# Performance work log

Measured on AMD Instinct MI355X. Metric: run time of the kernel, lower is better.

## Reference

```python
import jax, jax.numpy as jnp
import numpy as np

N_HEAD = 12

def setup_inputs() -> dict:
    key = jax.random.key(0)
    k1, k2, k3, k4, k5 = jax.random.split(key, 5)
    B, T, C = 16, 1024, 768
    s = 0.02
    return {
        "x": jax.random.normal(k1, (B, T, C), dtype=jnp.float32),
        "W_attn": jax.random.normal(k2, (C, 3 * C), dtype=jnp.float32) * s,
        "b_attn": jax.random.normal(k3, (3 * C,), dtype=jnp.float32) * s,
        "W_proj": jax.random.normal(k4, (C, C), dtype=jnp.float32) * s,
        "b_proj": jax.random.normal(k5, (C,), dtype=jnp.float32) * s,
    }

def reference(x, W_attn, b_attn, W_proj, b_proj):
    B, T, C = x.shape
    H = N_HEAD
    d = C // H
    qkv = x @ W_attn + b_attn                      # [B,T,3C]
    q, k, v = jnp.split(qkv, 3, axis=-1)
    # [B,H,T,d]
    q = q.reshape(B, T, H, d).transpose(0, 2, 1, 3)
    k = k.reshape(B, T, H, d).transpose(0, 2, 1, 3)
    v = v.reshape(B, T, H, d).transpose(0, 2, 1, 3)
    scale = 1.0 / jnp.sqrt(jnp.array(d, dtype=x.dtype))
    att = jnp.einsum('bhqd,bhkd->bhqk', q, k) * scale   # [B,H,T,T]
    causal = jnp.tril(jnp.ones((T, T), dtype=bool))
    att = jnp.where(causal[None, None], att, -jnp.inf)
    att = jax.nn.softmax(att, axis=-1)
    # dropout is identity in eval mode (p=0 for deterministic reference)
    y = jnp.einsum('bhqk,bhkd->bhqd', att, v)            # [B,H,T,d]
    y = y.transpose(0, 2, 1, 3).reshape(B, T, C)
    return y @ W_proj + b_proj
```

## Files before the change

kernel.cpp:

```cpp
#include <hip/hip_runtime.h>
#include <cstddef>


typedef __bf16 bf16_t;
typedef __bf16 bf16x4 __attribute__((ext_vector_type(4)));
typedef __bf16 bf16x8 __attribute__((ext_vector_type(8)));
typedef float  f32x4  __attribute__((ext_vector_type(4)));

#define MFMA16(a,b,c) __builtin_amdgcn_mfma_f32_16x16x32_bf16((a),(b),(c),0,0,0)
#define GLOAD16(gp, lp) \
  __builtin_amdgcn_global_load_lds((const __attribute__((address_space(1))) unsigned int*)(gp), \
                                   (__attribute__((address_space(3))) unsigned int*)(lp), 16, 0, 0)

#define SWZ(row, c) (((row) * 64) + ((((c) ^ ((row) & 7)) * 8)))

#define QSCALE 0.1803368801111f

__global__ __launch_bounds__(256)
void prep_kernel(const float* __restrict__ x, bf16_t* __restrict__ Xb,
                 const float* __restrict__ Wa, bf16_t* __restrict__ WaT,
                 const float* __restrict__ Wp, bf16_t* __restrict__ WpT)
{
    __shared__ bf16_t tile[32][33];
    const int bx = blockIdx.x;
    if (bx < 12288) {
        const size_t i = ((size_t)bx * 256 + threadIdx.x) * 4;
        float4 f = *(const float4*)(x + i);
        bf16x4 o = {(bf16_t)f.x, (bf16_t)f.y, (bf16_t)f.z, (bf16_t)f.w};
        *(bf16x4*)(Xb + i) = o;
        return;
    }
    const float* in;  bf16_t* out;  int R, Cn, c0, r0;
    if (bx < 14016) {
        const int t = bx - 12288;
        in = Wa; out = WaT; R = 768; Cn = 2304;
        c0 = (t % 72) * 32; r0 = (t / 72) * 32;
    } else {
        const int t = bx - 14016;
        in = Wp; out = WpT; R = 768; Cn = 768;
        c0 = (t % 24) * 32; r0 = (t / 24) * 32;
    }
    const int tx = threadIdx.x & 31, ty = threadIdx.x >> 5;
#pragma unroll
    for (int i = 0; i < 4; ++i)
        tile[ty + i*8][tx] = (bf16_t)in[(size_t)(r0 + ty + i*8) * Cn + c0 + tx];
    __syncthreads();
#pragma unroll
    for (int i = 0; i < 4; ++i)
        out[(size_t)(c0 + ty + i*8) * R + r0 + tx] = tile[tx][ty + i*8];
}

#define LGKM0() asm volatile("s_waitcnt lgkmcnt(0)" ::: "memory")
#define VMC(n)  asm volatile("s_waitcnt vmcnt(" #n ")" ::: "memory")
#define PBAR()  __builtin_amdgcn_s_barrier()
#define PRIO1() __builtin_amdgcn_s_setprio(1)
#define PRIO0() __builtin_amdgcn_s_setprio(0)

#define STAGE_HT(buf, kt, ht) do { \
    const int r0_ = w * 16 + (((ht) & 1) ? 128 : 0); \
    if ((ht) < 2) { \
        GLOAD16(WT + (size_t)(nt + r0_ + lr) * 768 + (kt) + lcs,     &Bs[buf][r0_ * 64]); \
        GLOAD16(WT + (size_t)(nt + r0_ + 8 + lr) * 768 + (kt) + lcs, &Bs[buf][(r0_ + 8) * 64]); \
    } else { \
        GLOAD16(Xb + (size_t)(mt + r0_ + lr) * 768 + (kt) + lcs,     &As[buf][r0_ * 64]); \
        GLOAD16(Xb + (size_t)(mt + r0_ + 8 + lr) * 768 + (kt) + lcs, &As[buf][(r0_ + 8) * 64]); \
    } \
} while (0)

#define RD_BX(dst, buf) do { \
    _Pragma("unroll") for (int j_ = 0; j_ < 4; ++j_) \
    _Pragma("unroll") for (int ks_ = 0; ks_ < 2; ++ks_) \
        (dst)[j_][ks_] = *(const bf16x8*)(&As[buf][SWZ(wc * 64 + j_ * 16 + lm, ks_ * 4 + lq)]); \
} while (0)

#define RD_AW(dst, buf, F0, NF) do { \
    _Pragma("unroll") for (int p_ = 0; p_ < (NF); ++p_) \
    _Pragma("unroll") for (int ks_ = 0; ks_ < 2; ++ks_) \
        (dst)[p_][ks_] = *(const bf16x8*)(&Bs[buf][SWZ(wr * 128 + ((F0) + p_) * 16 + lm, ks_ * 4 + lq)]); \
} while (0)

#define MFMA_Q(AW, BX, F0) do { \
    _Pragma("unroll") for (int ks_ = 0; ks_ < 2; ++ks_) \
    _Pragma("unroll") for (int p_ = 0; p_ < 2; ++p_) \
    _Pragma("unroll") for (int j_ = 0; j_ < 4; ++j_) \
        acc[(F0) + p_][j_] = MFMA16((AW)[p_][ks_], (BX)[j_][ks_], acc[(F0) + p_][j_]); \
} while (0)

__global__ __launch_bounds__(512)
void qkv_gemm8(const bf16_t* __restrict__ Xb, const bf16_t* __restrict__ WT,
               const float* __restrict__ bias,
               bf16_t* __restrict__ Qb, bf16_t* __restrict__ Kb, bf16_t* __restrict__ VT)
{
    __shared__ bf16_t As[2][256 * 64];
    __shared__ bf16_t Bs[2][256 * 64];
    const int tid = threadIdx.x;
    const int w = tid >> 6, l = tid & 63;
    const int lm = l & 15, lq = l >> 4;
    const int lr = l >> 3;
    const int lcs = ((l & 7) ^ lr) * 8;
    const int wr = w >> 2, wc = w & 3;

    const int g = blockIdx.x;
    const int gt = (g & 7) * 72 + (g >> 3);
    const int bm = gt / 9, bn = gt % 9;
    const int mt = bm * 256, nt = bn * 256;

    f32x4 acc[8][4];
    const f32x4 z4 = {0.f, 0.f, 0.f, 0.f};
#pragma unroll
    for (int i = 0; i < 8; ++i)
#pragma unroll
        for (int j = 0; j < 4; ++j) acc[i][j] = z4;

    bf16x8 bx0[4][2], bx1[4][2];
    bf16x8 aw0[2][2], aw12[4][2], aw3[2][2];

    STAGE_HT(0, 0, 0); STAGE_HT(0, 0, 1); STAGE_HT(0, 0, 2); STAGE_HT(0, 0, 3);
    STAGE_HT(1, 64, 0); STAGE_HT(1, 64, 1);
    VMC(4);
    PBAR();
    RD_BX(bx0, 0); RD_AW(aw0, 0, 0, 2);

#pragma unroll 1
    for (int it = 0; it < 5; ++it) {
        const int kv = it * 128 + 64, ku2 = kv + 64, kv2 = ku2 + 64;
        RD_AW(aw12, 0, 2, 4);
        STAGE_HT(1, kv, 2);
        PBAR(); LGKM0();
        PRIO1(); MFMA_Q(aw0, bx0, 0); PRIO0();
        PBAR();
        RD_AW(aw3, 0, 6, 2);
        STAGE_HT(1, kv, 3);
        PBAR(); LGKM0();
        PRIO1(); MFMA_Q(aw12, bx0, 2); PRIO0();
        PBAR();
        STAGE_HT(0, ku2, 0);
        PBAR();
        PRIO1(); MFMA_Q(&aw12[2], bx0, 4); PRIO0();
        VMC(2);
        PBAR();
        RD_BX(bx1, 1); RD_AW(aw0, 1, 0, 2);
        STAGE_HT(0, ku2, 1);
        PBAR(); LGKM0();
        PRIO1(); MFMA_Q(aw3, bx0, 6); PRIO0();
        PBAR();
        RD_AW(aw12, 1, 2, 4);
        STAGE_HT(0, ku2, 2);
        PBAR(); LGKM0();
        PRIO1(); MFMA_Q(aw0, bx1, 0); PRIO0();
        PBAR();
        RD_AW(aw3, 1, 6, 2);
        STAGE_HT(0, ku2, 3);
        PBAR(); LGKM0();
        PRIO1(); MFMA_Q(aw12, bx1, 2); PRIO0();
        PBAR();
        STAGE_HT(1, kv2, 0);
        PBAR();
        PRIO1(); MFMA_Q(&aw12[2], bx1, 4); PRIO0();
        VMC(2);
        PBAR();
        RD_BX(bx0, 0); RD_AW(aw0, 0, 0, 2);
        STAGE_HT(1, kv2, 1);
        PBAR(); LGKM0();
        PRIO1(); MFMA_Q(aw3, bx1, 6); PRIO0();
        PBAR();
    }

    RD_AW(aw12, 0, 2, 4);
    STAGE_HT(1, 704, 2);
    PBAR(); LGKM0();
    PRIO1(); MFMA_Q(aw0, bx0, 0); PRIO0();
    PBAR();
    RD_AW(aw3, 0, 6, 2);
    STAGE_HT(1, 704, 3);
    PBAR(); LGKM0();
    PRIO1(); MFMA_Q(aw12, bx0, 2); PRIO0();
    PBAR();
    PRIO1(); MFMA_Q(&aw12[2], bx0, 4); PRIO0();
    VMC(0);
    PBAR();
    RD_BX(bx1, 1); RD_AW(aw0, 1, 0, 2);
    MFMA_Q(aw3, bx0, 6);
    RD_AW(aw12, 1, 2, 4);
    LGKM0();
    MFMA_Q(aw0, bx1, 0);
    MFMA_Q(aw12, bx1, 2);
    RD_AW(aw3, 1, 6, 2);
    LGKM0();
    MFMA_Q(&aw12[2], bx1, 4);
    MFMA_Q(aw3, bx1, 6);

    const int which = (nt) / 768;
    const int b_ = mt >> 10;
    const int tb = (mt & 1023) + wc * 64;
    if (which == 2) {
#pragma unroll
        for (int f = 0; f < 8; ++f) {
            const int nglob = nt + wr * 128 + f * 16 + lq * 4;
            const int nin = nglob - 1536;
            const int h = nin >> 6, d0 = nin & 63;
            bf16_t* vt = VT + (size_t)(b_ * 12 + h) * 65536;
            const float4 bv = *(const float4*)(bias + nglob);
#pragma unroll
            for (int j = 0; j < 4; ++j) {
                const int t = tb + j * 16 + lm;
                f32x4 v = acc[f][j];
                vt[(size_t)(d0 + 0) * 1024 + t] = (bf16_t)(v[0] + bv.x);
                vt[(size_t)(d0 + 1) * 1024 + t] = (bf16_t)(v[1] + bv.y);
                vt[(size_t)(d0 + 2) * 1024 + t] = (bf16_t)(v[2] + bv.z);
                vt[(size_t)(d0 + 3) * 1024 + t] = (bf16_t)(v[3] + bv.w);
            }
        }
    } else {
        bf16_t* dst = (which == 0) ? Qb : Kb;
        const float qs = (which == 0) ? QSCALE : 1.0f;
#pragma unroll
        for (int f = 0; f < 8; ++f) {
            const int nglob = nt + wr * 128 + f * 16 + lq * 4;
            const int nin = nglob - which * 768;
            const int h = nin >> 6, d0 = nin & 63;
            const float4 bv = *(const float4*)(bias + nglob);
#pragma unroll
            for (int j = 0; j < 4; ++j) {
                const int t = tb + j * 16 + lm;
                f32x4 v = acc[f][j];
                bf16x4 o4 = {(bf16_t)((v[0] + bv.x) * qs), (bf16_t)((v[1] + bv.y) * qs),
                             (bf16_t)((v[2] + bv.z) * qs), (bf16_t)((v[3] + bv.w) * qs)};
                *(bf16x4*)(dst + ((size_t)(b_ * 12 + h) * 1024 + t) * 64 + d0) = o4;
            }
        }
    }
}

__global__ __launch_bounds__(256, 3)
void attn_kernel(const bf16_t* __restrict__ Qb, const bf16_t* __restrict__ Kb,
                 const bf16_t* __restrict__ VT, bf16_t* __restrict__ Y)
{
    __shared__ bf16_t Ks[2][64 * 64];
    __shared__ bf16_t Vs[2][64 * 64];
    __shared__ bf16_t Plds[4 * 16 * 72];
    const int tid = threadIdx.x;
    const int w = tid >> 6, l = tid & 63;
    const int lm = l & 15, lq = l >> 4;
    const int lr = l >> 3;
    const int lc8 = ((l & 7) ^ lr) * 8;
    const int xp = blockIdx.x;
    const int bh = blockIdx.y;
    const int loq = xp * 128, hiq = (7 - xp) * 128;

    int qmin[4];
    qmin[0] = loq + w * 32;      qmin[1] = qmin[0] + 16;
    qmin[2] = hiq + w * 32;      qmin[3] = qmin[2] + 16;

    const bf16_t* Kbase = Kb + (size_t)bh * 65536;
    const bf16_t* Vbase = VT + (size_t)bh * 65536;
    bf16_t* Pw = &Plds[w * 1152];
    const int r0a = w * 16, r0b = w * 16 + 8;

    bf16x8 bq[4][2];
#pragma unroll
    for (int m = 0; m < 4; ++m) {
        const bf16_t* Qp = Qb + ((size_t)bh * 1024 + qmin[m] + lm) * 64;
        bq[m][0] = *(const bf16x8*)(Qp + lq * 8);
        bq[m][1] = *(const bf16x8*)(Qp + 32 + lq * 8);
    }

    f32x4 O[4][4];
    float li[4] = {0.f, 0.f, 0.f, 0.f};
    const f32x4 z4 = {0.f, 0.f, 0.f, 0.f};
#pragma unroll
    for (int m = 0; m < 4; ++m)
#pragma unroll
        for (int s = 0; s < 4; ++s) O[m][s] = z4;

    const int kend = hiq + 64;

    GLOAD16(Kbase + (size_t)(r0a + lr) * 64 + lc8,   &Ks[0][r0a * 64]);
    GLOAD16(Kbase + (size_t)(r0b + lr) * 64 + lc8,   &Ks[0][r0b * 64]);
    GLOAD16(Vbase + (size_t)(r0a + lr) * 1024 + lc8, &Vs[0][r0a * 64]);
    GLOAD16(Vbase + (size_t)(r0b + lr) * 1024 + lc8, &Vs[0][r0b * 64]);
    __syncthreads();

    int cb = 0;
    for (int k0 = 0; k0 <= kend; k0 += 64) {
        const int nxt = cb ^ 1;
        if (k0 + 64 <= kend) {
            const int kn = k0 + 64;
            if (nxt) {
                GLOAD16(Kbase + (size_t)(kn + r0a + lr) * 64 + lc8,        &Ks[1][r0a * 64]);
                GLOAD16(Kbase + (size_t)(kn + r0b + lr) * 64 + lc8,        &Ks[1][r0b * 64]);
                GLOAD16(Vbase + (size_t)(r0a + lr) * 1024 + kn + lc8,      &Vs[1][r0a * 64]);
                GLOAD16(Vbase + (size_t)(r0b + lr) * 1024 + kn + lc8,      &Vs[1][r0b * 64]);
            } else {
                GLOAD16(Kbase + (size_t)(kn + r0a + lr) * 64 + lc8,        &Ks[0][r0a * 64]);
                GLOAD16(Kbase + (size_t)(kn + r0b + lr) * 64 + lc8,        &Ks[0][r0b * 64]);
                GLOAD16(Vbase + (size_t)(r0a + lr) * 1024 + kn + lc8,      &Vs[0][r0a * 64]);
                GLOAD16(Vbase + (size_t)(r0b + lr) * 1024 + kn + lc8,      &Vs[0][r0b * 64]);
            }
        }
        const bf16_t* Kc = Ks[cb];
        const bf16_t* Vc = Vs[cb];
#pragma unroll
        for (int m = 0; m < 4; ++m) {
            if (k0 > qmin[m] + 15) continue;
            f32x4 S[4];
#pragma unroll
            for (int s = 0; s < 4; ++s) S[s] = z4;
#pragma unroll
            for (int ks = 0; ks < 2; ++ks)
#pragma unroll
                for (int s = 0; s < 4; ++s) {
                    bf16x8 ak = *(const bf16x8*)(&Kc[SWZ(s * 16 + lm, ks * 4 + lq)]);
                    S[s] = MFMA16(ak, bq[m][ks], S[s]);
                }
            if (k0 + 63 > qmin[m]) {
                const int q = qmin[m] + lm;
#pragma unroll
                for (int s = 0; s < 4; ++s)
#pragma unroll
                    for (int rg = 0; rg < 4; ++rg)
                        if (k0 + s * 16 + lq * 4 + rg > q) S[s][rg] = -1e30f;
            }
            float ls = 0.f;
#pragma unroll
            for (int s = 0; s < 4; ++s)
#pragma unroll
                for (int rg = 0; rg < 4; ++rg) {
                    float pv = exp2f(S[s][rg]);
                    S[s][rg] = pv;
                    ls += pv;
                }
            li[m] += ls;
#pragma unroll
            for (int s = 0; s < 4; ++s) {
                bf16x4 p4 = {(bf16_t)S[s][0], (bf16_t)S[s][1],
                             (bf16_t)S[s][2], (bf16_t)S[s][3]};
                *(bf16x4*)(&Pw[lm * 72 + s * 16 + lq * 4]) = p4;
            }
#pragma unroll
            for (int ks = 0; ks < 2; ++ks) {
                bf16x8 bp = *(const bf16x8*)(&Pw[lm * 72 + ks * 32 + lq * 8]);
#pragma unroll
                for (int s = 0; s < 4; ++s) {
                    bf16x8 av = *(const bf16x8*)(&Vc[SWZ(s * 16 + lm, ks * 4 + lq)]);
                    O[m][s] = MFMA16(av, bp, O[m][s]);
                }
            }
        }
        __syncthreads();
        cb = nxt;
    }

    const int b = bh / 12, h = bh % 12;
#pragma unroll
    for (int m = 0; m < 4; ++m) {
        float s0 = li[m];
        s0 += __shfl_xor(s0, 16, 64);
        s0 += __shfl_xor(s0, 32, 64);
        const float inv = 1.f / s0;
        const size_t row = ((size_t)(b * 1024 + qmin[m] + lm)) * 768 + h * 64;
#pragma unroll
        for (int s = 0; s < 4; ++s) {
            bf16x4 y4 = {(bf16_t)(O[m][s][0] * inv), (bf16_t)(O[m][s][1] * inv),
                         (bf16_t)(O[m][s][2] * inv), (bf16_t)(O[m][s][3] * inv)};
            *(bf16x4*)(Y + row + s * 16 + lq * 4) = y4;
        }
    }
}

__global__ __launch_bounds__(256)
void proj_gemm(const bf16_t* __restrict__ A, const bf16_t* __restrict__ WT,
               const float* __restrict__ bias, float* __restrict__ out)
{
    __shared__ bf16_t As[128 * 64];
    __shared__ bf16_t Bs[128 * 64];
    const int tid = threadIdx.x;
    const int w = tid >> 6, l = tid & 63;
    const int lm = l & 15, lq = l >> 4;
    const int wy = w >> 1, wx = w & 1;
    const int lr = l >> 3;
    const int lcs = ((l & 7) ^ lr) * 8;
    const int nt = blockIdx.x * 128, mt = blockIdx.y * 128;

    f32x4 acc[4][4];
    const f32x4 z4 = {0.f, 0.f, 0.f, 0.f};
#pragma unroll
    for (int i = 0; i < 4; ++i)
#pragma unroll
        for (int j = 0; j < 4; ++j) acc[i][j] = z4;

    for (int kt = 0; kt < 768; kt += 64) {
#pragma unroll
        for (int p = 0; p < 4; ++p) {
            const int row = w * 32 + p * 8;
            GLOAD16(A  + (size_t)(mt + row + lr) * 768 + kt + lcs, &As[row * 64]);
            GLOAD16(WT + (size_t)(nt + row + lr) * 768 + kt + lcs, &Bs[row * 64]);
        }
        __syncthreads();
#pragma unroll
        for (int ks = 0; ks < 2; ++ks) {
            const int c = ks * 4 + lq;
            bf16x8 aw[4], bx[4];
#pragma unroll
            for (int i = 0; i < 4; ++i)
                aw[i] = *(const bf16x8*)(&Bs[SWZ(wx * 64 + i * 16 + lm, c)]);
#pragma unroll
            for (int j = 0; j < 4; ++j)
                bx[j] = *(const bf16x8*)(&As[SWZ(wy * 64 + j * 16 + lm, c)]);
#pragma unroll
            for (int i = 0; i < 4; ++i)
#pragma unroll
                for (int j = 0; j < 4; ++j)
                    acc[i][j] = MFMA16(aw[i], bx[j], acc[i][j]);
        }
        __syncthreads();
    }
#pragma unroll
    for (int i = 0; i < 4; ++i) {
        const int n0 = nt + wx * 64 + i * 16 + lq * 4;
        const float4 bv = *(const float4*)(bias + n0);
#pragma unroll
        for (int j = 0; j < 4; ++j) {
            const int t = mt + wy * 64 + j * 16 + lm;
            f32x4 v = acc[i][j];
            float4 o = {v[0] + bv.x, v[1] + bv.y, v[2] + bv.z, v[3] + bv.w};
            *(float4*)(out + (size_t)t * 768 + n0) = o;
        }
    }
}

extern "C" void kernel_launch(void* const* d_in, const int* in_sizes, int n_in,
                              void* d_out, int out_size, void* d_ws, size_t ws_size,
                              hipStream_t stream)
{
    const float* x      = (const float*)d_in[0];
    const float* W_attn = (const float*)d_in[1];
    const float* b_attn = (const float*)d_in[2];
    const float* W_proj = (const float*)d_in[3];
    const float* b_proj = (const float*)d_in[4];
    float* out = (float*)d_out;

    char* ws = (char*)d_ws;
    const size_t SZ = (size_t)16 * 12 * 1024 * 64 * 2;
    bf16_t* Qb  = (bf16_t*)(ws);
    bf16_t* Kb  = (bf16_t*)(ws + SZ);
    bf16_t* VT  = (bf16_t*)(ws + 3 * SZ);
    bf16_t* Yb  = (bf16_t*)(ws + 4 * SZ);
    bf16_t* Xb  = (bf16_t*)(ws + 4 * SZ);
    bf16_t* WaT = (bf16_t*)(ws + 5 * SZ);
    bf16_t* WpT = (bf16_t*)(ws + 5 * SZ + (size_t)2304 * 768 * 2);

    prep_kernel<<<14592, 256, 0, stream>>>(x, Xb, W_attn, WaT, W_proj, WpT);
    qkv_gemm8<<<576, 512, 0, stream>>>(Xb, WaT, b_attn, Qb, Kb, VT);
    attn_kernel<<<dim3(4, 192), 256, 0, stream>>>(Qb, Kb, VT, Yb);
    proj_gemm<<<dim3(6, 128), 256, 0, stream>>>(Yb, WpT, b_proj, out);
}
```

Baseline: 291.4 us.

## Split attention blocks per query tile and pass P via lane shuffles

```diff
diff --git a/kernel.cpp b/kernel.cpp
--- a/kernel.cpp
+++ b/kernel.cpp
@@ -3,6 +3,7 @@
 
 
 typedef __bf16 bf16_t;
+typedef __bf16 bf16x2 __attribute__((ext_vector_type(2)));
 typedef __bf16 bf16x4 __attribute__((ext_vector_type(4)));
 typedef __bf16 bf16x8 __attribute__((ext_vector_type(8)));
 typedef float  f32x4  __attribute__((ext_vector_type(4)));
@@ -232,13 +233,12 @@
     }
 }
 
-__global__ __launch_bounds__(256, 3)
+__global__ __launch_bounds__(256, 4)
 void attn_kernel(const bf16_t* __restrict__ Qb, const bf16_t* __restrict__ Kb,
                  const bf16_t* __restrict__ VT, bf16_t* __restrict__ Y)
 {
     __shared__ bf16_t Ks[2][64 * 64];
     __shared__ bf16_t Vs[2][64 * 64];
-    __shared__ bf16_t Plds[4 * 16 * 72];
     const int tid = threadIdx.x;
     const int w = tid >> 6, l = tid & 63;
     const int lm = l & 15, lq = l >> 4;
@@ -246,34 +246,33 @@
     const int lc8 = ((l & 7) ^ lr) * 8;
     const int xp = blockIdx.x;
     const int bh = blockIdx.y;
-    const int loq = xp * 128, hiq = (7 - xp) * 128;
-
-    int qmin[4];
-    qmin[0] = loq + w * 32;      qmin[1] = qmin[0] + 16;
-    qmin[2] = hiq + w * 32;      qmin[3] = qmin[2] + 16;
+    const int qb = xp * 128;
+
+    int qmin[2];
+    qmin[0] = qb + w * 32;  qmin[1] = qmin[0] + 16;
 
     const bf16_t* Kbase = Kb + (size_t)bh * 65536;
     const bf16_t* Vbase = VT + (size_t)bh * 65536;
-    bf16_t* Pw = &Plds[w * 1152];
     const int r0a = w * 16, r0b = w * 16 + 8;
 
-    bf16x8 bq[4][2];
-#pragma unroll
-    for (int m = 0; m < 4; ++m) {
+    bf16x8 bq[2][2];
+#pragma unroll
+    for (int m = 0; m < 2; ++m) {
         const bf16_t* Qp = Qb + ((size_t)bh * 1024 + qmin[m] + lm) * 64;
         bq[m][0] = *(const bf16x8*)(Qp + lq * 8);
         bq[m][1] = *(const bf16x8*)(Qp + 32 + lq * 8);
     }
 
-    f32x4 O[4][4];
-    float li[4] = {0.f, 0.f, 0.f, 0.f};
+    f32x4 O[2][4];
+    float li[2] = {0.f, 0.f};
     const f32x4 z4 = {0.f, 0.f, 0.f, 0.f};
 #pragma unroll
-    for (int m = 0; m < 4; ++m)
+    for (int m = 0; m < 2; ++m)
 #pragma unroll
         for (int s = 0; s < 4; ++s) O[m][s] = z4;
 
-    const int kend = hiq + 64;
+    const int kend = qb + 64;
+    const int sb = lm + 32 * (lq & 1);
 
     GLOAD16(Kbase + (size_t)(r0a + lr) * 64 + lc8,   &Ks[0][r0a * 64]);
     GLOAD16(Kbase + (size_t)(r0b + lr) * 64 + lc8,   &Ks[0][r0b * 64]);
@@ -301,7 +300,7 @@
         const bf16_t* Kc = Ks[cb];
         const bf16_t* Vc = Vs[cb];
 #pragma unroll
-        for (int m = 0; m < 4; ++m) {
+        for (int m = 0; m < 2; ++m) {
             if (k0 > qmin[m] + 15) continue;
             f32x4 S[4];
 #pragma unroll
@@ -331,19 +330,27 @@
                     ls += pv;
                 }
             li[m] += ls;
-#pragma unroll
-            for (int s = 0; s < 4; ++s) {
-                bf16x4 p4 = {(bf16_t)S[s][0], (bf16_t)S[s][1],
-                             (bf16_t)S[s][2], (bf16_t)S[s][3]};
-                *(bf16x4*)(&Pw[lm * 72 + s * 16 + lq * 4]) = p4;
-            }
+
 #pragma unroll
             for (int ks = 0; ks < 2; ++ks) {
-                bf16x8 bp = *(const bf16x8*)(&Pw[lm * 72 + ks * 32 + lq * 8]);
+                union { bf16x2 h; int u; } c0, c1, c2, c3;
+                c0.h = bf16x2{(bf16_t)S[2*ks][0],     (bf16_t)S[2*ks][1]};
+                c1.h = bf16x2{(bf16_t)S[2*ks][2],     (bf16_t)S[2*ks][3]};
+                c2.h = bf16x2{(bf16_t)S[2*ks + 1][0], (bf16_t)S[2*ks + 1][1]};
+                c3.h = bf16x2{(bf16_t)S[2*ks + 1][2], (bf16_t)S[2*ks + 1][3]};
+                const int a0 = __shfl(c0.u, sb, 64),      b0 = __shfl(c2.u, sb, 64);
+                const int a1 = __shfl(c1.u, sb, 64),      b1 = __shfl(c3.u, sb, 64);
+                const int a2 = __shfl(c0.u, sb + 16, 64), b2 = __shfl(c2.u, sb + 16, 64);
+                const int a3 = __shfl(c1.u, sb + 16, 64), b3 = __shfl(c3.u, sb + 16, 64);
+                union { int u[4]; bf16x8 v; } bp;
+                bp.u[0] = (lq < 2) ? a0 : b0;
+                bp.u[1] = (lq < 2) ? a1 : b1;
+                bp.u[2] = (lq < 2) ? a2 : b2;
+                bp.u[3] = (lq < 2) ? a3 : b3;
 #pragma unroll
                 for (int s = 0; s < 4; ++s) {
                     bf16x8 av = *(const bf16x8*)(&Vc[SWZ(s * 16 + lm, ks * 4 + lq)]);
-                    O[m][s] = MFMA16(av, bp, O[m][s]);
+                    O[m][s] = MFMA16(av, bp.v, O[m][s]);
                 }
             }
         }
@@ -353,7 +360,7 @@
 
     const int b = bh / 12, h = bh % 12;
 #pragma unroll
-    for (int m = 0; m < 4; ++m) {
+    for (int m = 0; m < 2; ++m) {
         float s0 = li[m];
         s0 += __shfl_xor(s0, 16, 64);
         s0 += __shfl_xor(s0, 32, 64);
@@ -452,6 +459,6 @@
 
     prep_kernel<<<14592, 256, 0, stream>>>(x, Xb, W_attn, WaT, W_proj, WpT);
     qkv_gemm8<<<576, 512, 0, stream>>>(Xb, WaT, b_attn, Qb, Kb, VT);
-    attn_kernel<<<dim3(4, 192), 256, 0, stream>>>(Qb, Kb, VT, Yb);
+    attn_kernel<<<dim3(8, 192), 256, 0, stream>>>(Qb, Kb, VT, Yb);
     proj_gemm<<<dim3(6, 128), 256, 0, stream>>>(Yb, WpT, b_proj, out);
 }
```

Result: slower. 323.0 us (+10.9%).
